# Performance work log

Measured on AMD Instinct MI355X. Metric: run time of the kernel, lower is better.

## Reference

```python
import jax, jax.numpy as jnp
import numpy as np

TINY = float(np.finfo(np.float32).tiny)


def setup_inputs() -> dict:
    key = jax.random.key(0)
    ks = jax.random.split(key, 8)
    B, T, Qd, Vd, D = 32, 8192, 512, 256, 128
    query = jax.random.normal(ks[0], (B, Qd), jnp.float32)
    value = jax.random.normal(ks[1], (B, T, Vd), jnp.float32)
    previous_alignment = jax.random.uniform(ks[2], (B, T), jnp.float32)
    # normalize to a valid alignment distribution per row (as in real decoding)
    previous_alignment = previous_alignment / jnp.sum(previous_alignment, axis=-1, keepdims=True)
    Wq = jax.random.normal(ks[3], (Qd, D), jnp.float32) * 0.02
    bq = jnp.zeros((D,), jnp.float32)
    Wv = jax.random.normal(ks[4], (Vd, D), jnp.float32) * 0.02
    bv = jnp.zeros((D,), jnp.float32)
    attention_v = jax.random.normal(ks[5], (D,), jnp.float32) * 0.1
    score_bias = jnp.zeros((), jnp.float32)
    return dict(query=query, value=value, previous_alignment=previous_alignment,
                Wq=Wq, bq=bq, Wv=Wv, bv=bv, attention_v=attention_v,
                score_bias=score_bias)


def reference(query, value, previous_alignment, Wq, bq, Wv, bv, attention_v, score_bias):
    # Query/Value dense projections (3-input form: key == projected value)
    q = query @ Wq + bq                                   # [B, D]
    v = value @ Wv + bv                                   # [B, T, D]
    # Bahdanau additive score: sum(v_att * tanh(q + k), -1) + bias -> [B, T]
    score = jnp.einsum('d,btd->bt', attention_v, jnp.tanh(q[:, None, :] + v)) + score_bias
    # Monotonic attention (recursive form, parallelized via cumsum/cumprod)
    p = jax.nn.sigmoid(score)                             # p_choose_i
    logs = jnp.log(jnp.clip(1.0 - p, TINY, 1.0))
    # exclusive safe cumprod of (1 - p): exp(exclusive cumsum of log)
    cp = jnp.exp(jnp.cumsum(logs, axis=-1) - logs)        # [B, T]
    alignment = p * cp * jnp.cumsum(
        previous_alignment / jnp.clip(cp, 1e-10, 1.0), axis=-1)
    # context = alignment @ projected value -> [B, D]
    context = jnp.einsum('bt,btd->bd', alignment, v)
    return context, alignment
```

## Files before the change

### kernel.cpp

```cpp
#include <hip/hip_runtime.h>
#include <hip/hip_bf16.h>
#include <math.h>

#define BB   32
#define TT_  8192
#define QD   512
#define VD   256
#define DD   128
#define TINYF 1.17549435e-38f

#define TTILE 64
#define CCH   32

#define TSPEC 512
#define TSPEC_TILES (TSPEC / TTILE)
#define TSPEC_CHUNKS (TSPEC / 256)

__global__ __launch_bounds__(256) void k_score(
    const float* __restrict__ value, const float* __restrict__ query,
    const float* __restrict__ Wq, const float* __restrict__ bq,
    const float* __restrict__ Wv, const float* __restrict__ bv,
    const float* __restrict__ attv, const float* __restrict__ sbias,
    float* __restrict__ score, int t_tile_base, const int* __restrict__ flags) {
  int b = blockIdx.y;
  if (flags && flags[b] == 0) return;
  int tid = threadIdx.x;

  __shared__ float qrow[QD];
  __shared__ float qpart[2][DD];
  __shared__ float qsh[DD];
  qrow[tid]       = query[b * QD + tid];
  qrow[tid + 256] = query[b * QD + tid + 256];
  __syncthreads();
  {
    int h = tid >> 7, d = tid & 127;
    const float* wq = Wq + (size_t)(h * 256) * DD + d;
    const float* qr = qrow + h * 256;
    float acc = 0.f;
    #pragma unroll 8
    for (int c = 0; c < 256; ++c) acc = fmaf(qr[c], wq[(size_t)c * DD], acc);
    qpart[h][d] = acc;
  }
  __syncthreads();
  if (tid < DD) qsh[tid] = qpart[0][tid] + qpart[1][tid] + bq[tid] + bv[tid];
  __syncthreads();

  int t0 = (t_tile_base + blockIdx.x) * TTILE;
  int dq = tid & 31;
  int tq = tid >> 5;

  __shared__ float WvL[CCH * DD];
  __shared__ float valT[CCH * 68];

  float acc[8][4];
  #pragma unroll
  for (int i = 0; i < 8; ++i)
    #pragma unroll
    for (int j = 0; j < 4; ++j) acc[i][j] = 0.f;

  const float* vbase = value + ((size_t)b * TT_ + t0) * VD;

  for (int c0 = 0; c0 < VD; c0 += CCH) {
    const float4* wsrc = (const float4*)(Wv + (size_t)c0 * DD);
    float4* wdst = (float4*)WvL;
    #pragma unroll
    for (int k = 0; k < 4; ++k) wdst[tid + 256 * k] = wsrc[tid + 256 * k];
    #pragma unroll
    for (int k = 0; k < 2; ++k) {
      int id = tid * 2 + k;
      int tt = id >> 3;
      int c4 = id & 7;
      float4 vv = *(const float4*)(vbase + (size_t)tt * VD + c0 + c4 * 4);
      int cr = c4 * 4;
      valT[(cr + 0) * 68 + tt] = vv.x;
      valT[(cr + 1) * 68 + tt] = vv.y;
      valT[(cr + 2) * 68 + tt] = vv.z;
      valT[(cr + 3) * 68 + tt] = vv.w;
    }
    __syncthreads();
    #pragma unroll 4
    for (int cc = 0; cc < CCH; ++cc) {
      const float4 wv  = *(const float4*)(&WvL[cc * DD + dq * 4]);
      const float4 va0 = *(const float4*)(&valT[cc * 68 + tq * 8]);
      const float4 va1 = *(const float4*)(&valT[cc * 68 + tq * 8 + 4]);
      float va[8] = {va0.x, va0.y, va0.z, va0.w, va1.x, va1.y, va1.z, va1.w};
      #pragma unroll
      for (int i = 0; i < 8; ++i) {
        acc[i][0] = fmaf(va[i], wv.x, acc[i][0]);
        acc[i][1] = fmaf(va[i], wv.y, acc[i][1]);
        acc[i][2] = fmaf(va[i], wv.z, acc[i][2]);
        acc[i][3] = fmaf(va[i], wv.w, acc[i][3]);
      }
    }
    __syncthreads();
  }

  float sb = sbias[0];
  float qd[4], av[4];
  #pragma unroll
  for (int j = 0; j < 4; ++j) {
    int d = dq * 4 + j;
    qd[j] = qsh[d];
    av[j] = attv[d];
  }
  #pragma unroll
  for (int i = 0; i < 8; ++i) {
    float s = 0.f;
    #pragma unroll
    for (int j = 0; j < 4; ++j) {
      float x = qd[j] + acc[i][j];
      s += av[j] * tanhf(x);
    }
    #pragma unroll
    for (int m = 16; m >= 1; m >>= 1) s += __shfl_xor(s, m, 64);
    if (dq == 0) score[(size_t)b * TT_ + t0 + tq * 8 + i] = s + sb;
  }
}

__global__ __launch_bounds__(256) void k_fused(
    const float* __restrict__ score, const float* __restrict__ prev,
    const float* __restrict__ value, const float* __restrict__ Wv,
    const float* __restrict__ bv,
    float* __restrict__ align_out, float* __restrict__ ctx,
    float* __restrict__ suma, float* __restrict__ carryL,
    float* __restrict__ carryD, float* __restrict__ uws,
    int* __restrict__ flags) {
  int b = blockIdx.x, tid = threadIdx.x;
  int lane = tid & 63, w = tid >> 6;
  __shared__ float wsA[4], wsB[4], wsS[4];
  __shared__ float aL[256], uL[256];
  const size_t base = (size_t)b * TT_;

  float cL = 0.f, cD = 0.f, sacc = 0.f, uacc = 0.f;

  for (int ch = 0; ch < TSPEC_CHUNKS; ++ch) {
    int t = ch * 256 + tid;
    float s = score[base + t];
    float p  = 1.f / (1.f + expf(-s));
    float om = 1.f / (1.f + expf(s));
    float l = logf(fmaxf(om, TINYF));

    float inc = l;
    #pragma unroll
    for (int o = 1; o < 64; o <<= 1) {
      float n = __shfl_up(inc, o, 64);
      if (lane >= o) inc += n;
    }
    if (lane == 63) wsA[w] = inc;
    __syncthreads();
    float off = 0.f;
    #pragma unroll
    for (int j = 0; j < 4; ++j) if (j < w) off += wsA[j];
    float totA = wsA[0] + wsA[1] + wsA[2] + wsA[3];
    float cp = expf(cL + off + inc - l);
    float den = prev[base + t] / fminf(fmaxf(cp, 1e-10f), 1.f);

    float inc2 = den;
    #pragma unroll
    for (int o = 1; o < 64; o <<= 1) {
      float n = __shfl_up(inc2, o, 64);
      if (lane >= o) inc2 += n;
    }
    if (lane == 63) wsB[w] = inc2;
    __syncthreads();
    float off2 = 0.f;
    #pragma unroll
    for (int j = 0; j < 4; ++j) if (j < w) off2 += wsB[j];
    float totB = wsB[0] + wsB[1] + wsB[2] + wsB[3];

    float a = p * cp * (cD + off2 + inc2);
    align_out[base + t] = a;
    sacc += a;
    aL[tid] = a;
    __syncthreads();

    const float* vp = value + (base + (size_t)ch * 256) * VD + tid;
    #pragma unroll 8
    for (int tt = 0; tt < 256; ++tt)
      uacc = fmaf(aL[tt], vp[(size_t)tt * VD], uacc);

    cL += totA; cD += totB;
    __syncthreads();
  }

  #pragma unroll
  for (int o = 32; o >= 1; o >>= 1) sacc += __shfl_xor(sacc, o, 64);
  if (lane == 0) wsS[w] = sacc;
  __syncthreads();
  float stot = wsS[0] + wsS[1] + wsS[2] + wsS[3];

  int fb = __builtin_amdgcn_readfirstlane((expf(cL) != 0.f) ? 1 : 0);

  if (fb) {
    if (tid == 0) { flags[b] = 1; suma[b] = stot; carryL[b] = cL; carryD[b] = cD; }
    uws[b * VD + tid] = uacc;
  } else {
    if (tid == 0) { flags[b] = 0; suma[b] = stot; }
    float4 z = make_float4(0.f, 0.f, 0.f, 0.f);
    float4* dst = (float4*)(align_out + base + TSPEC);
    for (int i = tid; i < (TT_ - TSPEC) / 4; i += 256) dst[i] = z;
  }

  uL[tid] = uacc;
  __syncthreads();
  if (!fb && tid < DD) {
    float c = stot * bv[tid];
    #pragma unroll 8
    for (int cc = 0; cc < VD; ++cc) c = fmaf(uL[cc], Wv[cc * DD + tid], c);
    ctx[b * DD + tid] = c;
  }
}

__global__ __launch_bounds__(256) void k_scan1(
    const float* __restrict__ score, const float* __restrict__ prev,
    float* __restrict__ align_out, float* __restrict__ suma,
    const float* __restrict__ carryL, const float* __restrict__ carryD,
    const int* __restrict__ flags) {
  int b = blockIdx.x, tid = threadIdx.x;
  if (flags[b] == 0) return;
  int lane = tid & 63, w = tid >> 6;
  __shared__ float wsA[4], wsB[4];
  float cL = carryL[b], cD = carryD[b], sacc = suma[b];
  const size_t base = (size_t)b * TT_;

  for (int ch = TSPEC_CHUNKS; ch < TT_ / 256; ++ch) {
    int t = ch * 256 + tid;
    float s = score[base + t];
    float p  = 1.f / (1.f + expf(-s));
    float om = 1.f / (1.f + expf(s));
    float l = logf(fmaxf(om, TINYF));

    float inc = l;
    #pragma unroll
    for (int o = 1; o < 64; o <<= 1) {
      float n = __shfl_up(inc, o, 64);
      if (lane >= o) inc += n;
    }
    if (lane == 63) wsA[w] = inc;
    __syncthreads();
    float off = 0.f;
    #pragma unroll
    for (int j = 0; j < 4; ++j) if (j < w) off += wsA[j];
    float totA = wsA[0] + wsA[1] + wsA[2] + wsA[3];
    float cp = expf(cL + off + inc - l);
    float den = prev[base + t] / fminf(fmaxf(cp, 1e-10f), 1.f);

    float inc2 = den;
    #pragma unroll
    for (int o = 1; o < 64; o <<= 1) {
      float n = __shfl_up(inc2, o, 64);
      if (lane >= o) inc2 += n;
    }
    if (lane == 63) wsB[w] = inc2;
    __syncthreads();
    float off2 = 0.f;
    #pragma unroll
    for (int j = 0; j < 4; ++j) if (j < w) off2 += wsB[j];
    float totB = wsB[0] + wsB[1] + wsB[2] + wsB[3];

    float a = p * cp * (cD + off2 + inc2);
    align_out[base + t] = a;
    sacc += a;
    cL += totA; cD += totB;
    __syncthreads();
  }

  #pragma unroll
  for (int o = 32; o >= 1; o >>= 1) sacc += __shfl_xor(sacc, o, 64);
  if (lane == 0) wsA[w] = sacc;
  __syncthreads();
  if (tid == 0) suma[b] = wsA[0] + wsA[1] + wsA[2] + wsA[3];
}

__global__ __launch_bounds__(256) void k_uctx_fb(
    const float* __restrict__ value, const float* __restrict__ align,
    const float* __restrict__ Wv, const float* __restrict__ bv,
    const float* __restrict__ suma, const float* __restrict__ uws,
    float* __restrict__ ctx, const int* __restrict__ flags) {
  int b = blockIdx.x, tid = threadIdx.x;
  if (flags[b] == 0) return;
  __shared__ float aL[256];
  __shared__ float uL[256];
  __shared__ int any;
  const size_t base = (size_t)b * TT_;
  float acc = uws[b * VD + tid];
  for (int ch = TSPEC_CHUNKS; ch < TT_ / 256; ++ch) {
    if (tid == 0) any = 0;
    __syncthreads();
    float a = align[base + ch * 256 + tid];
    aL[tid] = a;
    if (a != 0.f) any = 1;
    __syncthreads();
    if (any) {
      const float* vp = value + (base + (size_t)ch * 256) * VD + tid;
      #pragma unroll 8
      for (int t = 0; t < 256; ++t) acc = fmaf(aL[t], vp[(size_t)t * VD], acc);
    }
    __syncthreads();
  }
  uL[tid] = acc;
  __syncthreads();
  if (tid < DD) {
    float c = suma[b] * bv[tid];
    #pragma unroll 8
    for (int cc = 0; cc < VD; ++cc) c = fmaf(uL[cc], Wv[cc * DD + tid], c);
    ctx[b * DD + tid] = c;
  }
}

extern "C" void kernel_launch(void* const* d_in, const int* in_sizes, int n_in,
                              void* d_out, int out_size, void* d_ws, size_t ws_size,
                              hipStream_t stream) {
  const float* query = (const float*)d_in[0];
  const float* value = (const float*)d_in[1];
  const float* prev  = (const float*)d_in[2];
  const float* Wq    = (const float*)d_in[3];
  const float* bq    = (const float*)d_in[4];
  const float* Wv    = (const float*)d_in[5];
  const float* bv    = (const float*)d_in[6];
  const float* attv  = (const float*)d_in[7];
  const float* sbias = (const float*)d_in[8];

  float* ctx_out   = (float*)d_out;
  float* align_out = (float*)d_out + BB * DD;

  float* ws = (float*)d_ws;
  float* score  = ws;
  float* suma   = ws + 262144;
  float* carryL = ws + 262176;
  float* carryD = ws + 262208;
  int*   flags  = (int*)(ws + 262240);
  float* uws    = ws + 262272;

  k_score<<<dim3(TSPEC_TILES, BB), 256, 0, stream>>>(
      value, query, Wq, bq, Wv, bv, attv, sbias, score, 0, nullptr);

  k_fused<<<BB, 256, 0, stream>>>(score, prev, value, Wv, bv, align_out,
                                  ctx_out, suma, carryL, carryD, uws, flags);

  k_score<<<dim3((TT_ - TSPEC) / TTILE, BB), 256, 0, stream>>>(
      value, query, Wq, bq, Wv, bv, attv, sbias, score, TSPEC_TILES, flags);
  k_scan1<<<BB, 256, 0, stream>>>(score, prev, align_out, suma,
                                  carryL, carryD, flags);
  k_uctx_fb<<<BB, 256, 0, stream>>>(value, align_out, Wv, bv, suma, uws,
                                    ctx_out, flags);
}
```

Before: 381.1 us.

## Process speculative prefix in one 512-thread pass and merge fallback tail kernels

The fused prefix kernel now runs with 512 threads and handles the whole 512-step speculative prefix in one pass instead of two sequential 256-step chunks. The value-weighted accumulation and the final Wv projection are each split across two thread halves and combined through shared memory. The fallback scan and context kernels are merged into one kernel that computes alignment and accumulates the weighted values in the same loop, removing one launch and one re-read of the alignment. The cost is more threads and shared memory per block, and an extra reduction step.

After: 368.2 us. 3.4% less time.

```diff
diff --git a/kernel.cpp b/kernel.cpp
--- a/kernel.cpp
+++ b/kernel.cpp
@@ -14,7 +14,6 @@
 
 #define TSPEC 512
 #define TSPEC_TILES (TSPEC / TTILE)
-#define TSPEC_CHUNKS (TSPEC / 256)
 
 __global__ __launch_bounds__(256) void k_score(
     const float* __restrict__ value, const float* __restrict__ query,
@@ -117,7 +116,7 @@
   }
 }
 
-__global__ __launch_bounds__(256) void k_fused(
+__global__ __launch_bounds__(512) void k_fused(
     const float* __restrict__ score, const float* __restrict__ prev,
     const float* __restrict__ value, const float* __restrict__ Wv,
     const float* __restrict__ bv,
@@ -127,13 +126,115 @@
     int* __restrict__ flags) {
   int b = blockIdx.x, tid = threadIdx.x;
   int lane = tid & 63, w = tid >> 6;
-  __shared__ float wsA[4], wsB[4], wsS[4];
-  __shared__ float aL[256], uL[256];
+  __shared__ float wsA[8], wsB[8], wsS[8];
+  __shared__ float aL[TSPEC];
+  __shared__ float uhalf[512];
+  __shared__ float uL[VD];
+  __shared__ float cpart[256];
   const size_t base = (size_t)b * TT_;
 
-  float cL = 0.f, cD = 0.f, sacc = 0.f, uacc = 0.f;
-
-  for (int ch = 0; ch < TSPEC_CHUNKS; ++ch) {
+  float s = score[base + tid];
+  float p  = 1.f / (1.f + expf(-s));
+  float om = 1.f / (1.f + expf(s));
+  float l = logf(fmaxf(om, TINYF));
+
+  float inc = l;
+  #pragma unroll
+  for (int o = 1; o < 64; o <<= 1) {
+    float n = __shfl_up(inc, o, 64);
+    if (lane >= o) inc += n;
+  }
+  if (lane == 63) wsA[w] = inc;
+  __syncthreads();
+  float off = 0.f, totA = 0.f;
+  #pragma unroll
+  for (int j = 0; j < 8; ++j) { float x = wsA[j]; totA += x; if (j < w) off += x; }
+  float cp = expf(off + inc - l);
+  float den = prev[base + tid] / fminf(fmaxf(cp, 1e-10f), 1.f);
+
+  float inc2 = den;
+  #pragma unroll
+  for (int o = 1; o < 64; o <<= 1) {
+    float n = __shfl_up(inc2, o, 64);
+    if (lane >= o) inc2 += n;
+  }
+  if (lane == 63) wsB[w] = inc2;
+  __syncthreads();
+  float off2 = 0.f, totB = 0.f;
+  #pragma unroll
+  for (int j = 0; j < 8; ++j) { float x = wsB[j]; totB += x; if (j < w) off2 += x; }
+
+  float a = p * cp * (off2 + inc2);
+  align_out[base + tid] = a;
+  aL[tid] = a;
+
+  float sacc = a;
+  #pragma unroll
+  for (int o = 32; o >= 1; o >>= 1) sacc += __shfl_xor(sacc, o, 64);
+  if (lane == 0) wsS[w] = sacc;
+  __syncthreads();
+  float stot = 0.f;
+  #pragma unroll
+  for (int j = 0; j < 8; ++j) stot += wsS[j];
+
+  int c = tid & (VD - 1);
+  int half = tid >> 8;
+  const float* vp = value + (base + (size_t)half * 256) * VD + c;
+  const float* ap = aL + half * 256;
+  float uacc = 0.f;
+  #pragma unroll 8
+  for (int tt = 0; tt < 256; ++tt) uacc = fmaf(ap[tt], vp[(size_t)tt * VD], uacc);
+  uhalf[tid] = uacc;
+  __syncthreads();
+  if (tid < VD) uL[tid] = uhalf[tid] + uhalf[tid + VD];
+  __syncthreads();
+
+  int fb = __builtin_amdgcn_readfirstlane((expf(totA) != 0.f) ? 1 : 0);
+
+  if (fb) {
+    if (tid == 0) { flags[b] = 1; suma[b] = stot; carryL[b] = totA; carryD[b] = totB; }
+    if (tid < VD) uws[b * VD + tid] = uL[tid];
+  } else {
+    if (tid == 0) flags[b] = 0;
+    float4 z = make_float4(0.f, 0.f, 0.f, 0.f);
+    float4* dst = (float4*)(align_out + base + TSPEC);
+    for (int i = tid; i < (TT_ - TSPEC) / 4; i += 512) dst[i] = z;
+  }
+
+  if (!fb && tid < 256) {
+    int d = tid & 127, h = tid >> 7;
+    float cval = (h == 0) ? stot * bv[d] : 0.f;
+    const float* wp = Wv + (size_t)(h * 128) * DD + d;
+    const float* up = uL + h * 128;
+    #pragma unroll 8
+    for (int cc = 0; cc < 128; ++cc) cval = fmaf(up[cc], wp[(size_t)cc * DD], cval);
+    cpart[tid] = cval;
+  }
+  __syncthreads();
+  if (!fb && tid < DD) ctx[b * DD + tid] = cpart[tid] + cpart[tid + 128];
+}
+
+__global__ __launch_bounds__(256) void k_tail_fb(
+    const float* __restrict__ score, const float* __restrict__ prev,
+    const float* __restrict__ value, const float* __restrict__ Wv,
+    const float* __restrict__ bv, const float* __restrict__ suma_in,
+    const float* __restrict__ carryL, const float* __restrict__ carryD,
+    const float* __restrict__ uws,
+    float* __restrict__ align_out, float* __restrict__ ctx,
+    const int* __restrict__ flags) {
+  int b = blockIdx.x, tid = threadIdx.x;
+  if (flags[b] == 0) return;
+  int lane = tid & 63, w = tid >> 6;
+  __shared__ float wsA[4], wsB[4];
+  __shared__ float aL[256];
+  __shared__ float uL[256];
+  __shared__ int any;
+  float cL = carryL[b], cD = carryD[b];
+  float sacc = (tid == 0) ? suma_in[b] : 0.f;
+  float uacc = uws[b * VD + tid];
+  const size_t base = (size_t)b * TT_;
+
+  for (int ch = TSPEC / 256; ch < TT_ / 256; ++ch) {
     int t = ch * 256 + tid;
     float s = score[base + t];
     float p  = 1.f / (1.f + expf(-s));
@@ -147,6 +248,7 @@
       if (lane >= o) inc += n;
     }
     if (lane == 63) wsA[w] = inc;
+    if (tid == 0) any = 0;
     __syncthreads();
     float off = 0.f;
     #pragma unroll
@@ -172,136 +274,28 @@
     align_out[base + t] = a;
     sacc += a;
     aL[tid] = a;
-    __syncthreads();
-
-    const float* vp = value + (base + (size_t)ch * 256) * VD + tid;
-    #pragma unroll 8
-    for (int tt = 0; tt < 256; ++tt)
-      uacc = fmaf(aL[tt], vp[(size_t)tt * VD], uacc);
-
-    cL += totA; cD += totB;
-    __syncthreads();
-  }
-
-  #pragma unroll
-  for (int o = 32; o >= 1; o >>= 1) sacc += __shfl_xor(sacc, o, 64);
-  if (lane == 0) wsS[w] = sacc;
-  __syncthreads();
-  float stot = wsS[0] + wsS[1] + wsS[2] + wsS[3];
-
-  int fb = __builtin_amdgcn_readfirstlane((expf(cL) != 0.f) ? 1 : 0);
-
-  if (fb) {
-    if (tid == 0) { flags[b] = 1; suma[b] = stot; carryL[b] = cL; carryD[b] = cD; }
-    uws[b * VD + tid] = uacc;
-  } else {
-    if (tid == 0) { flags[b] = 0; suma[b] = stot; }
-    float4 z = make_float4(0.f, 0.f, 0.f, 0.f);
-    float4* dst = (float4*)(align_out + base + TSPEC);
-    for (int i = tid; i < (TT_ - TSPEC) / 4; i += 256) dst[i] = z;
-  }
-
-  uL[tid] = uacc;
-  __syncthreads();
-  if (!fb && tid < DD) {
-    float c = stot * bv[tid];
-    #pragma unroll 8
-    for (int cc = 0; cc < VD; ++cc) c = fmaf(uL[cc], Wv[cc * DD + tid], c);
-    ctx[b * DD + tid] = c;
-  }
-}
-
-__global__ __launch_bounds__(256) void k_scan1(
-    const float* __restrict__ score, const float* __restrict__ prev,
-    float* __restrict__ align_out, float* __restrict__ suma,
-    const float* __restrict__ carryL, const float* __restrict__ carryD,
-    const int* __restrict__ flags) {
-  int b = blockIdx.x, tid = threadIdx.x;
-  if (flags[b] == 0) return;
-  int lane = tid & 63, w = tid >> 6;
-  __shared__ float wsA[4], wsB[4];
-  float cL = carryL[b], cD = carryD[b], sacc = suma[b];
-  const size_t base = (size_t)b * TT_;
-
-  for (int ch = TSPEC_CHUNKS; ch < TT_ / 256; ++ch) {
-    int t = ch * 256 + tid;
-    float s = score[base + t];
-    float p  = 1.f / (1.f + expf(-s));
-    float om = 1.f / (1.f + expf(s));
-    float l = logf(fmaxf(om, TINYF));
-
-    float inc = l;
-    #pragma unroll
-    for (int o = 1; o < 64; o <<= 1) {
-      float n = __shfl_up(inc, o, 64);
-      if (lane >= o) inc += n;
-    }
-    if (lane == 63) wsA[w] = inc;
-    __syncthreads();
-    float off = 0.f;
-    #pragma unroll
-    for (int j = 0; j < 4; ++j) if (j < w) off += wsA[j];
-    float totA = wsA[0] + wsA[1] + wsA[2] + wsA[3];
-    float cp = expf(cL + off + inc - l);
-    float den = prev[base + t] / fminf(fmaxf(cp, 1e-10f), 1.f);
-
-    float inc2 = den;
-    #pragma unroll
-    for (int o = 1; o < 64; o <<= 1) {
-      float n = __shfl_up(inc2, o, 64);
-      if (lane >= o) inc2 += n;
-    }
-    if (lane == 63) wsB[w] = inc2;
-    __syncthreads();
-    float off2 = 0.f;
-    #pragma unroll
-    for (int j = 0; j < 4; ++j) if (j < w) off2 += wsB[j];
-    float totB = wsB[0] + wsB[1] + wsB[2] + wsB[3];
-
-    float a = p * cp * (cD + off2 + inc2);
-    align_out[base + t] = a;
-    sacc += a;
-    cL += totA; cD += totB;
-    __syncthreads();
-  }
-
-  #pragma unroll
-  for (int o = 32; o >= 1; o >>= 1) sacc += __shfl_xor(sacc, o, 64);
-  if (lane == 0) wsA[w] = sacc;
-  __syncthreads();
-  if (tid == 0) suma[b] = wsA[0] + wsA[1] + wsA[2] + wsA[3];
-}
-
-__global__ __launch_bounds__(256) void k_uctx_fb(
-    const float* __restrict__ value, const float* __restrict__ align,
-    const float* __restrict__ Wv, const float* __restrict__ bv,
-    const float* __restrict__ suma, const float* __restrict__ uws,
-    float* __restrict__ ctx, const int* __restrict__ flags) {
-  int b = blockIdx.x, tid = threadIdx.x;
-  if (flags[b] == 0) return;
-  __shared__ float aL[256];
-  __shared__ float uL[256];
-  __shared__ int any;
-  const size_t base = (size_t)b * TT_;
-  float acc = uws[b * VD + tid];
-  for (int ch = TSPEC_CHUNKS; ch < TT_ / 256; ++ch) {
-    if (tid == 0) any = 0;
-    __syncthreads();
-    float a = align[base + ch * 256 + tid];
-    aL[tid] = a;
     if (a != 0.f) any = 1;
     __syncthreads();
+
     if (any) {
       const float* vp = value + (base + (size_t)ch * 256) * VD + tid;
       #pragma unroll 8
-      for (int t = 0; t < 256; ++t) acc = fmaf(aL[t], vp[(size_t)t * VD], acc);
-    }
-    __syncthreads();
-  }
-  uL[tid] = acc;
+      for (int tt = 0; tt < 256; ++tt) uacc = fmaf(aL[tt], vp[(size_t)tt * VD], uacc);
+    }
+    cL += totA; cD += totB;
+    __syncthreads();
+  }
+
+  #pragma unroll
+  for (int o = 32; o >= 1; o >>= 1) sacc += __shfl_xor(sacc, o, 64);
+  if (lane == 0) wsA[w] = sacc;
+  __syncthreads();
+  float stot = wsA[0] + wsA[1] + wsA[2] + wsA[3];
+
+  uL[tid] = uacc;
   __syncthreads();
   if (tid < DD) {
-    float c = suma[b] * bv[tid];
+    float c = stot * bv[tid];
     #pragma unroll 8
     for (int cc = 0; cc < VD; ++cc) c = fmaf(uL[cc], Wv[cc * DD + tid], c);
     ctx[b * DD + tid] = c;
@@ -335,13 +329,12 @@
   k_score<<<dim3(TSPEC_TILES, BB), 256, 0, stream>>>(
       value, query, Wq, bq, Wv, bv, attv, sbias, score, 0, nullptr);
 
-  k_fused<<<BB, 256, 0, stream>>>(score, prev, value, Wv, bv, align_out,
+  k_fused<<<BB, 512, 0, stream>>>(score, prev, value, Wv, bv, align_out,
                                   ctx_out, suma, carryL, carryD, uws, flags);
 
   k_score<<<dim3((TT_ - TSPEC) / TTILE, BB), 256, 0, stream>>>(
       value, query, Wq, bq, Wv, bv, attv, sbias, score, TSPEC_TILES, flags);
-  k_scan1<<<BB, 256, 0, stream>>>(score, prev, align_out, suma,
-                                  carryL, carryD, flags);
-  k_uctx_fb<<<BB, 256, 0, stream>>>(value, align_out, Wv, bv, suma, uws,
-                                    ctx_out, flags);
+  k_tail_fb<<<BB, 256, 0, stream>>>(score, prev, value, Wv, bv, suma,
+                                    carryL, carryD, uws, align_out, ctx_out,
+                                    flags);
 }
```
